# Kernel tuning notes

Measured on AMD Instinct MI355X. Metric: run time of the kernel, lower is better.

The kernel has to match this reference:

```python
import jax, jax.numpy as jnp
import numpy as np

B, T, I, H, O = 64, 1024, 256, 512, 128


def setup_inputs() -> dict:
    key = jax.random.key(0)
    ks = jax.random.split(key, 12)
    s = 1.0 / np.sqrt(H)  # PyTorch LSTM init: U(-1/sqrt(H), 1/sqrt(H))
    u = lambda k, shape: jax.random.uniform(k, shape, jnp.float32, -s, s)
    return {
        "inputs": jax.random.normal(ks[0], (B, T, I), jnp.float32),
        "W_ih_f": u(ks[1], (4 * H, I)),
        "W_hh_f": u(ks[2], (4 * H, H)),
        "b_ih_f": u(ks[3], (4 * H,)),
        "b_hh_f": u(ks[4], (4 * H,)),
        "W_ih_b": u(ks[5], (4 * H, I)),
        "W_hh_b": u(ks[6], (4 * H, H)),
        "b_ih_b": u(ks[7], (4 * H,)),
        "b_hh_b": u(ks[8], (4 * H,)),
        "W_out": u(ks[9], (O, 2 * H)),
        "b_out": u(ks[10], (O,)),
    }


def _lstm_dir(inputs, W_ih, W_hh, b_ih, b_hh, reverse):
    # Precompute input contribution for all timesteps: [B,T,4H] -> [T,B,4H]
    xg = jnp.einsum("bti,gi->btg", inputs, W_ih) + b_ih + b_hh
    xg = jnp.swapaxes(xg, 0, 1)
    b = inputs.shape[0]
    h0 = jnp.zeros((b, H), inputs.dtype)
    c0 = jnp.zeros((b, H), inputs.dtype)

    def step(carry, x_t):
        h, c = carry
        gates = x_t + h @ W_hh.T  # [B,4H], PyTorch gate order i,f,g,o
        i, f, g, o = jnp.split(gates, 4, axis=-1)
        i = jax.nn.sigmoid(i)
        f = jax.nn.sigmoid(f)
        g = jnp.tanh(g)
        o = jax.nn.sigmoid(o)
        c = f * c + i * g
        h = o * jnp.tanh(c)
        return (h, c), h

    (hT, cT), hs = jax.lax.scan(step, (h0, c0), xg, reverse=reverse)
    return jnp.swapaxes(hs, 0, 1), hT, cT  # hs: [B,T,H]


def reference(inputs, W_ih_f, W_hh_f, b_ih_f, b_hh_f,
              W_ih_b, W_hh_b, b_ih_b, b_hh_b, W_out, b_out):
    y_f, h_f, c_f = _lstm_dir(inputs, W_ih_f, W_hh_f, b_ih_f, b_hh_f, False)
    y_b, h_b, c_b = _lstm_dir(inputs, W_ih_b, W_hh_b, b_ih_b, b_hh_b, True)
    y = jnp.concatenate([y_f, y_b], axis=-1)            # [B,T,2H]
    out = jnp.einsum("bth,oh->bto", y, W_out) + b_out    # [B,T,O]
    h_n = jnp.stack([h_f, h_b])                          # [2,B,H]
    c_n = jnp.stack([c_f, c_b])                          # [2,B,H]
    return out, h_n, c_n
```

## Files before the change

### kernel.cpp

```cpp
#include <hip/hip_runtime.h>
#include <stdint.h>

#define T_LEN 1024
#define B_SZ  64
#define I_SZ  256
#define H_SZ  512
#define O_SZ  128

#define FLAG_OFF 0ull
#define HB_OFF  65536ull
#define Y_OFF   327680ull
#define XBF_OFF 134545408ull
#define MEMSET_BYTES 327680ull

typedef __attribute__((ext_vector_type(8))) short short8;
typedef __attribute__((ext_vector_type(4))) float f32x4;

__device__ __forceinline__ unsigned short f2bf(float f) {
  unsigned u = __float_as_uint(f);
  u += 0x7fffu + ((u >> 16) & 1u);
  return (unsigned short)(u >> 16);
}
__device__ __forceinline__ ushort4 cvt4(float4 v) {
  ushort4 p;
  p.x = f2bf(v.x); p.y = f2bf(v.y); p.z = f2bf(v.z); p.w = f2bf(v.w);
  return p;
}
__device__ __forceinline__ float sigm(float x) { return 1.0f / (1.0f + __expf(-x)); }
__device__ __forceinline__ float tanh_f(float x) { return 1.0f - 2.0f / (1.0f + __expf(2.0f * x)); }

__global__ void __launch_bounds__(256) cvt_x(const float* __restrict__ x,
                                             unsigned short* __restrict__ xb) {
  size_t i = ((size_t)blockIdx.x * 256 + threadIdx.x) * 8;
  float4 a = *(const float4*)(x + i);
  float4 b = *(const float4*)(x + i + 4);
  *(ushort4*)(xb + i)     = cvt4(a);
  *(ushort4*)(xb + i + 4) = cvt4(b);
}

__global__ void __launch_bounds__(512, 2)
lstm_scan(const unsigned short* __restrict__ xbf,
          const float* __restrict__ WihF, const float* __restrict__ WhhF,
          const float* __restrict__ bihF, const float* __restrict__ bhhF,
          const float* __restrict__ WihB, const float* __restrict__ WhhB,
          const float* __restrict__ bihB, const float* __restrict__ bhhB,
          unsigned char* __restrict__ ws, float* __restrict__ out)
{
  __shared__ unsigned short xs[2][16][264];
  __shared__ unsigned short hs[16][520];
  __shared__ float gbuf[4][16][36];
  __shared__ float cst[16][36];

  const int tid  = threadIdx.x;
  const int lane = tid & 63;
  const int wave = tid >> 6;
  const int nl   = lane & 15;
  const int q16  = lane >> 4;

  const int wg   = blockIdx.x;
  const int d    = wg >> 6;
  const int b0   = ((wg >> 4) & 3) * 16;
  const int u0   = (wg & 15) * 32;
  const int grp  = wg >> 4;
  const int wgid = wg & 15;

  const float* Wih = d ? WihB : WihF;
  const float* Whh = d ? WhhB : WhhF;
  const float* bih = d ? bihB : bihF;
  const float* bhh = d ? bhhB : bhhF;

  const int gate = wave >> 1;
  const int usub = (wave & 1) * 16;

  short8 wfrag[24];
  {
    const int row = gate * H_SZ + u0 + usub + nl;
    const float* wi = Wih + (size_t)row * I_SZ;
    const float* wh = Whh + (size_t)row * H_SZ;
#pragma unroll
    for (int kk = 0; kk < 24; ++kk) {
      const float* src = (kk < 8) ? (wi + kk * 32 + q16 * 8)
                                  : (wh + (kk - 8) * 32 + q16 * 8);
      float4 v0 = ((const float4*)src)[0];
      float4 v1 = ((const float4*)src)[1];
      short8 w;
      w[0] = (short)f2bf(v0.x); w[1] = (short)f2bf(v0.y);
      w[2] = (short)f2bf(v0.z); w[3] = (short)f2bf(v0.w);
      w[4] = (short)f2bf(v1.x); w[5] = (short)f2bf(v1.y);
      w[6] = (short)f2bf(v1.z); w[7] = (short)f2bf(v1.w);
      wfrag[kk] = w;
    }
  }
  const float bias = bih[gate * H_SZ + u0 + usub + nl] + bhh[gate * H_SZ + u0 + usub + nl];

  cst[tid >> 5][tid & 31] = 0.0f;

  unsigned* flags  = (unsigned*)(ws + FLAG_OFF);
  unsigned* hbuf32 = (unsigned*)(ws + HB_OFF);
  unsigned* ybuf32 = (unsigned*)(ws + Y_OFF);
  unsigned* hs32   = (unsigned*)hs;

  const int sm = tid >> 5, sseg = tid & 31;

  {
    const int t0 = d ? (T_LEN - 1) : 0;
    uint4 a = *(const uint4*)(xbf + ((size_t)(b0 + sm) * T_LEN + t0) * I_SZ + sseg * 8);
    *(uint4*)(&xs[0][sm][sseg * 8]) = a;
  }
  __syncthreads();
  f32x4 xacc = {0.f, 0.f, 0.f, 0.f};
  {
    const unsigned short* xr = &xs[0][nl][q16 * 8];
#pragma unroll
    for (int kk = 0; kk < 8; ++kk) {
      short8 a = *(const short8*)(xr + kk * 32);
      xacc = __builtin_amdgcn_mfma_f32_16x16x32_bf16(a, wfrag[kk], xacc, 0, 0, 0);
    }
  }
  uint4 px;
  {
    const int t1 = d ? (T_LEN - 2) : 1;
    px = *(const uint4*)(xbf + ((size_t)(b0 + sm) * T_LEN + t1) * I_SZ + sseg * 8);
  }

  for (int s = 0; s < T_LEN; ++s) {
    const int t   = d ? (T_LEN - 1 - s) : s;
    const int cur = s & 1, nxt = cur ^ 1;
    const int rb  = cur ^ 1, wb = cur;

    if (s > 0) {
      const unsigned tgt = (unsigned)s;
      const unsigned* fl = flags + grp * 16;
      for (;;) {
        unsigned f = (lane < 16)
          ? __hip_atomic_load(fl + lane, __ATOMIC_RELAXED, __HIP_MEMORY_SCOPE_AGENT)
          : tgt;
        if (__all((int)(f >= tgt))) break;
      }
    }

    {
      unsigned hv[8];
      const unsigned* hb = hbuf32 + (size_t)((rb * 2 + d) * B_SZ + b0) * 256;
#pragma unroll
      for (int j = 0; j < 8; ++j)
        hv[j] = __hip_atomic_load(hb + j * 512 + tid, __ATOMIC_RELAXED, __HIP_MEMORY_SCOPE_AGENT);
      if (s < T_LEN - 1)
        *(uint4*)(&xs[nxt][sm][sseg * 8]) = px;
#pragma unroll
      for (int j = 0; j < 8; ++j) {
        int lin = j * 512 + tid;
        hs32[(lin >> 8) * 260 + (lin & 255)] = hv[j];
      }
    }
    __syncthreads();

    f32x4 acc0 = xacc, acc1 = {0.f, 0.f, 0.f, 0.f};
    {
      const unsigned short* ar = &hs[nl][q16 * 8];
#pragma unroll
      for (int kk = 0; kk < 16; kk += 2) {
        short8 a0 = *(const short8*)(ar + kk * 32);
        short8 a1 = *(const short8*)(ar + (kk + 1) * 32);
        acc0 = __builtin_amdgcn_mfma_f32_16x16x32_bf16(a0, wfrag[8 + kk], acc0, 0, 0, 0);
        acc1 = __builtin_amdgcn_mfma_f32_16x16x32_bf16(a1, wfrag[9 + kk], acc1, 0, 0, 0);
      }
      acc0 += acc1;
    }

#pragma unroll
    for (int r = 0; r < 4; ++r) {
      float v = acc0[r] + bias;
      v = (gate == 2) ? tanh_f(v) : sigm(v);
      gbuf[gate][q16 * 4 + r][usub + nl] = v;
    }
    __syncthreads();

    unsigned packed; size_t yi;
    {
      int m = tid >> 5, n = tid & 31;
      float gi = gbuf[0][m][n], gf = gbuf[1][m][n];
      float gg = gbuf[2][m][n], go = gbuf[3][m][n];
      float c = gf * cst[m][n] + gi * gg;
      cst[m][n] = c;
      float h = go * tanh_f(c);
      unsigned hbits = f2bf(h);
      unsigned other = __shfl_xor(hbits, 1);
      packed = hbits | (other << 16);
      yi = ((size_t)(b0 + m) * T_LEN + t) * 512 + (d * H_SZ + u0 + n) / 2;
      if ((tid & 1) == 0) {
        size_t hi = (size_t)((wb * 2 + d) * B_SZ + b0 + m) * 256 + (u0 + n) / 2;
        __hip_atomic_store(hbuf32 + hi, packed, __ATOMIC_RELAXED, __HIP_MEMORY_SCOPE_AGENT);
      }
      if (s == T_LEN - 1) {
        size_t hi = (size_t)(d * B_SZ + b0 + m) * H_SZ + u0 + n;
        out[8388608ull + hi] = h;
        out[8388608ull + 65536ull + hi] = c;
      }
    }

    if (s < T_LEN - 1) {
      __builtin_amdgcn_s_waitcnt(0);
      __syncthreads();
      if (tid == 0)
        __hip_atomic_store(flags + grp * 16 + wgid, (unsigned)(s + 1),
                           __ATOMIC_RELAXED, __HIP_MEMORY_SCOPE_AGENT);
    }

    if ((tid & 1) == 0)
      ybuf32[yi] = packed;

    if (s < T_LEN - 1) {
      if (s + 2 < T_LEN) {
        const int t2 = d ? (T_LEN - 3 - s) : (s + 2);
        px = *(const uint4*)(xbf + ((size_t)(b0 + sm) * T_LEN + t2) * I_SZ + sseg * 8);
      }
      f32x4 xa = {0.f, 0.f, 0.f, 0.f};
      const unsigned short* xr = &xs[nxt][nl][q16 * 8];
#pragma unroll
      for (int kk = 0; kk < 8; ++kk) {
        short8 a = *(const short8*)(xr + kk * 32);
        xa = __builtin_amdgcn_mfma_f32_16x16x32_bf16(a, wfrag[kk], xa, 0, 0, 0);
      }
      xacc = xa;
    }
  }
}

__global__ void __launch_bounds__(256, 1)
proj(const unsigned short* __restrict__ y, const float* __restrict__ Wout,
     const float* __restrict__ bout, float* __restrict__ out)
{
  __shared__ unsigned short ys[128 * 264];
  __shared__ unsigned short wst[128 * 264];

  const int tid  = threadIdx.x;
  const int wave = tid >> 6;
  const int lane = tid & 63;
  const int nl   = lane & 15;
  const int q16  = lane >> 4;
  const int m0   = blockIdx.x * 128;

  f32x4 acc[2][8];
#pragma unroll
  for (int a = 0; a < 2; ++a)
#pragma unroll
    for (int b = 0; b < 8; ++b) acc[a][b] = (f32x4){0.f, 0.f, 0.f, 0.f};

  for (int k0 = 0; k0 < 1024; k0 += 256) {
    {
      int r = tid >> 1, half = tid & 1;
      const uint4* src = (const uint4*)(y + (size_t)(m0 + r) * 1024 + k0 + half * 128);
      uint4* dst = (uint4*)(ys + r * 264 + half * 128);
#pragma unroll
      for (int q = 0; q < 16; ++q) dst[q] = src[q];
    }
    {
      int r = tid >> 1, half = tid & 1;
      const float4* src = (const float4*)(Wout + (size_t)r * 1024 + k0 + half * 128);
      unsigned short* wd = wst + r * 264 + half * 128;
#pragma unroll
      for (int q = 0; q < 32; ++q) *(ushort4*)(wd + q * 4) = cvt4(src[q]);
    }
    __syncthreads();

#pragma unroll
    for (int kk = 0; kk < 8; ++kk) {
      const int ko = kk * 32 + q16 * 8;
      short8 bfr[8];
#pragma unroll
      for (int nt = 0; nt < 8; ++nt)
        bfr[nt] = *(const short8*)(wst + (nt * 16 + nl) * 264 + ko);
#pragma unroll
      for (int mtt = 0; mtt < 2; ++mtt) {
        short8 a = *(const short8*)(ys + ((wave * 2 + mtt) * 16 + nl) * 264 + ko);
#pragma unroll
        for (int nt = 0; nt < 8; ++nt)
          acc[mtt][nt] = __builtin_amdgcn_mfma_f32_16x16x32_bf16(a, bfr[nt], acc[mtt][nt], 0, 0, 0);
      }
    }
    __syncthreads();
  }

#pragma unroll
  for (int mtt = 0; mtt < 2; ++mtt) {
#pragma unroll
    for (int nt = 0; nt < 8; ++nt) {
      int col = nt * 16 + nl;
      float bo = bout[col];
      int rowb = m0 + (wave * 2 + mtt) * 16 + q16 * 4;
#pragma unroll
      for (int r = 0; r < 4; ++r)
        out[(size_t)(rowb + r) * O_SZ + col] = acc[mtt][nt][r] + bo;
    }
  }
}

extern "C" void kernel_launch(void* const* d_in, const int* in_sizes, int n_in,
                              void* d_out, int out_size, void* d_ws, size_t ws_size,
                              hipStream_t stream) {
  const float* x    = (const float*)d_in[0];
  const float* WihF = (const float*)d_in[1];
  const float* WhhF = (const float*)d_in[2];
  const float* bihF = (const float*)d_in[3];
  const float* bhhF = (const float*)d_in[4];
  const float* WihB = (const float*)d_in[5];
  const float* WhhB = (const float*)d_in[6];
  const float* bihB = (const float*)d_in[7];
  const float* bhhB = (const float*)d_in[8];
  const float* Wout = (const float*)d_in[9];
  const float* bout = (const float*)d_in[10];
  float* out = (float*)d_out;
  unsigned char* ws = (unsigned char*)d_ws;

  hipMemsetAsync(ws, 0, (size_t)MEMSET_BYTES, stream);
  cvt_x<<<8192, 256, 0, stream>>>(x, (unsigned short*)(ws + XBF_OFF));
  lstm_scan<<<128, 512, 0, stream>>>((const unsigned short*)(ws + XBF_OFF),
                                     WihF, WhhF, bihF, bhhF,
                                     WihB, WhhB, bihB, bhhB,
                                     ws, out);
  proj<<<512, 256, 0, stream>>>((const unsigned short*)(ws + Y_OFF), Wout, bout, out);
}
```

Measured before the change: 3.798 ms.

## Replace flag-based step barrier with per-element tagged hidden-state words

Each hidden-state value is now stored as a 32-bit word that packs the bf16 value with the step tag, so consumers poll the data itself instead of a separate per-group flag array. This removes the waitcnt, extra __syncthreads and flag store/poll round trip on every timestep of the recurrence. In exchange the h exchange buffer doubles in size, readers load twice as many words and unpack them, and correctness relies on 32-bit atomic stores making value and tag visible together.

New measurement: 3.259 ms. 1.17x faster.

```diff
diff --git a/kernel.cpp b/kernel.cpp
--- a/kernel.cpp
+++ b/kernel.cpp
@@ -7,11 +7,10 @@
 #define H_SZ  512
 #define O_SZ  128
 
-#define FLAG_OFF 0ull
-#define HB_OFF  65536ull
-#define Y_OFF   327680ull
-#define XBF_OFF 134545408ull
-#define MEMSET_BYTES 327680ull
+#define HB_OFF  0ull
+#define Y_OFF   1048576ull
+#define XBF_OFF 135266304ull
+#define MEMSET_BYTES 1048576ull
 
 typedef __attribute__((ext_vector_type(8))) short short8;
 typedef __attribute__((ext_vector_type(4))) float f32x4;
@@ -57,12 +56,10 @@
   const int nl   = lane & 15;
   const int q16  = lane >> 4;
 
-  const int wg   = blockIdx.x;
-  const int d    = wg >> 6;
-  const int b0   = ((wg >> 4) & 3) * 16;
-  const int u0   = (wg & 15) * 32;
-  const int grp  = wg >> 4;
-  const int wgid = wg & 15;
+  const int wg = blockIdx.x;
+  const int d  = wg >> 6;
+  const int b0 = ((wg >> 4) & 3) * 16;
+  const int u0 = (wg & 15) * 32;
 
   const float* Wih = d ? WihB : WihF;
   const float* Whh = d ? WhhB : WhhF;
@@ -95,7 +92,6 @@
 
   cst[tid >> 5][tid & 31] = 0.0f;
 
-  unsigned* flags  = (unsigned*)(ws + FLAG_OFF);
   unsigned* hbuf32 = (unsigned*)(ws + HB_OFF);
   unsigned* ybuf32 = (unsigned*)(ws + Y_OFF);
   unsigned* hs32   = (unsigned*)hs;
@@ -128,30 +124,40 @@
     const int cur = s & 1, nxt = cur ^ 1;
     const int rb  = cur ^ 1, wb = cur;
 
-    if (s > 0) {
-      const unsigned tgt = (unsigned)s;
-      const unsigned* fl = flags + grp * 16;
+    unsigned wlo[8], whi[8];
+    const unsigned* hb = hbuf32 + (size_t)((rb * 2 + d) * B_SZ + b0) * 512;
+#pragma unroll
+    for (int j = 0; j < 8; ++j) {
+      int lin2 = j * 512 + tid;
+      int m = lin2 >> 8, p = lin2 & 255;
+      wlo[j] = __hip_atomic_load(hb + m * 512 + 2 * p,     __ATOMIC_RELAXED, __HIP_MEMORY_SCOPE_AGENT);
+      whi[j] = __hip_atomic_load(hb + m * 512 + 2 * p + 1, __ATOMIC_RELAXED, __HIP_MEMORY_SCOPE_AGENT);
+    }
+    if (s < T_LEN - 1)
+      *(uint4*)(&xs[nxt][sm][sseg * 8]) = px;
+    {
+      const unsigned tag = (unsigned)s;
       for (;;) {
-        unsigned f = (lane < 16)
-          ? __hip_atomic_load(fl + lane, __ATOMIC_RELAXED, __HIP_MEMORY_SCOPE_AGENT)
-          : tgt;
-        if (__all((int)(f >= tgt))) break;
-      }
-    }
-
-    {
-      unsigned hv[8];
-      const unsigned* hb = hbuf32 + (size_t)((rb * 2 + d) * B_SZ + b0) * 256;
-#pragma unroll
-      for (int j = 0; j < 8; ++j)
-        hv[j] = __hip_atomic_load(hb + j * 512 + tid, __ATOMIC_RELAXED, __HIP_MEMORY_SCOPE_AGENT);
-      if (s < T_LEN - 1)
-        *(uint4*)(&xs[nxt][sm][sseg * 8]) = px;
-#pragma unroll
-      for (int j = 0; j < 8; ++j) {
-        int lin = j * 512 + tid;
-        hs32[(lin >> 8) * 260 + (lin & 255)] = hv[j];
-      }
+        unsigned bad = 0;
+#pragma unroll
+        for (int j = 0; j < 8; ++j)
+          bad |= (((wlo[j] ^ tag) | (whi[j] ^ tag)) & 0xffffu) ? (1u << j) : 0u;
+        if (!bad) break;
+#pragma unroll
+        for (int j = 0; j < 8; ++j)
+          if (bad & (1u << j)) {
+            int lin2 = j * 512 + tid;
+            int m = lin2 >> 8, p = lin2 & 255;
+            wlo[j] = __hip_atomic_load(hb + m * 512 + 2 * p,     __ATOMIC_RELAXED, __HIP_MEMORY_SCOPE_AGENT);
+            whi[j] = __hip_atomic_load(hb + m * 512 + 2 * p + 1, __ATOMIC_RELAXED, __HIP_MEMORY_SCOPE_AGENT);
+          }
+      }
+    }
+#pragma unroll
+    for (int j = 0; j < 8; ++j) {
+      int lin2 = j * 512 + tid;
+      int m = lin2 >> 8, p = lin2 & 255;
+      hs32[m * 260 + p] = (wlo[j] >> 16) | (whi[j] & 0xffff0000u);
     }
     __syncthreads();
 
@@ -176,7 +182,6 @@
     }
     __syncthreads();
 
-    unsigned packed; size_t yi;
     {
       int m = tid >> 5, n = tid & 31;
       float gi = gbuf[0][m][n], gf = gbuf[1][m][n];
@@ -185,12 +190,14 @@
       cst[m][n] = c;
       float h = go * tanh_f(c);
       unsigned hbits = f2bf(h);
+      __hip_atomic_store(hbuf32 + (size_t)((wb * 2 + d) * B_SZ + b0 + m) * 512 + u0 + n,
+                         (hbits << 16) | (unsigned)(s + 1),
+                         __ATOMIC_RELAXED, __HIP_MEMORY_SCOPE_AGENT);
       unsigned other = __shfl_xor(hbits, 1);
-      packed = hbits | (other << 16);
-      yi = ((size_t)(b0 + m) * T_LEN + t) * 512 + (d * H_SZ + u0 + n) / 2;
       if ((tid & 1) == 0) {
-        size_t hi = (size_t)((wb * 2 + d) * B_SZ + b0 + m) * 256 + (u0 + n) / 2;
-        __hip_atomic_store(hbuf32 + hi, packed, __ATOMIC_RELAXED, __HIP_MEMORY_SCOPE_AGENT);
+        unsigned packed = hbits | (other << 16);
+        size_t yi = ((size_t)(b0 + m) * T_LEN + t) * 512 + (d * H_SZ + u0 + n) / 2;
+        ybuf32[yi] = packed;
       }
       if (s == T_LEN - 1) {
         size_t hi = (size_t)(d * B_SZ + b0 + m) * H_SZ + u0 + n;
@@ -198,17 +205,6 @@
         out[8388608ull + 65536ull + hi] = c;
       }
     }
-
-    if (s < T_LEN - 1) {
-      __builtin_amdgcn_s_waitcnt(0);
-      __syncthreads();
-      if (tid == 0)
-        __hip_atomic_store(flags + grp * 16 + wgid, (unsigned)(s + 1),
-                           __ATOMIC_RELAXED, __HIP_MEMORY_SCOPE_AGENT);
-    }
-
-    if ((tid & 1) == 0)
-      ybuf32[yi] = packed;
 
     if (s < T_LEN - 1) {
       if (s + 2 < T_LEN) {
```
